# Kernel tuning notes

Hardware: AMD Instinct MI355X
Metric: run time of the kernel (lower is better)

The kernel has to match this reference:

```python
import jax, jax.numpy as jnp
import numpy as np

N = 400000      # total atoms across batch of molecules
E = 1600000     # directed edges (avg degree 4)
G = 4096        # number of graphs (molecules)
F_IN = 78       # atomic feature size
H = 128         # gnn hidden dims (gnn_0 = gnn_1 = 128)
FF0, FF1 = 256, 128


def _lin(k, fan_in, fan_out):
    return jax.random.normal(k, (fan_in, fan_out), jnp.float32) / np.sqrt(fan_in).astype(np.float32)


def setup_inputs() -> dict:
    key = jax.random.key(0)
    ks = jax.random.split(key, 10)
    x = jax.random.normal(ks[0], (N, F_IN), jnp.float32)
    edge_index = jax.random.randint(ks[1], (2, E), 0, N, dtype=jnp.int64)
    # sorted graph ids, guaranteed non-empty segments (empty segment -> -inf under max pool)
    batch = (jnp.arange(N, dtype=jnp.int64) * G) // N
    return {
        'x': x, 'edge_index': edge_index, 'batch': batch,
        'W0': _lin(ks[2], F_IN, H), 'b0': jnp.zeros((H,), jnp.float32),
        'W1': _lin(ks[3], H, H),    'b1': jnp.zeros((H,), jnp.float32),
        'Wf0': _lin(ks[4], H, FF0), 'bf0': jnp.zeros((FF0,), jnp.float32),
        'Wf1': _lin(ks[5], FF0, FF1), 'bf1': jnp.zeros((FF1,), jnp.float32),
    }


def _gcn_conv(h, W, b, src, dst, dinv):
    # GCNConv with add_self_loops=True, symmetric normalization.
    hw = h @ W                                     # [N, out]
    norm = dinv[src] * dinv[dst]                   # [E]
    msg = hw[src] * norm[:, None]                  # gather + scale
    agg = jax.ops.segment_sum(msg, dst, num_segments=h.shape[0])
    agg = agg + hw * (dinv * dinv)[:, None]        # self-loop contribution
    return agg + b


def reference(x, edge_index, batch, W0, b0, W1, b1, Wf0, bf0, Wf1, bf1):
    src, dst = edge_index[0], edge_index[1]
    # degree of A + I computed at target nodes (PyG gcn_norm uses col)
    deg = jax.ops.segment_sum(jnp.ones((E,), x.dtype), dst, num_segments=N) + 1.0
    dinv = jax.lax.rsqrt(deg)

    h = jax.nn.relu(_gcn_conv(x, W0, b0, src, dst, dinv))
    h = jax.nn.relu(_gcn_conv(h, W1, b1, src, dst, dinv))

    g = jax.ops.segment_max(h, batch, num_segments=G)   # global max pool [G, H]

    g = jax.nn.relu(g @ Wf0 + bf0)   # dropout is identity in eval
    g = jax.nn.relu(g @ Wf1 + bf1)
    return g
```

## Files before the change

kernel.cpp:

```cpp
#include <hip/hip_runtime.h>
#include <cstdint>
#include <cstddef>

#define NATOMS 400000
#define NEDGES 1600000
#define NGRAPH 4096
#define F_INN  78
#define HDIM   128
#define FF0D   256
#define FF1D   128

typedef __attribute__((ext_vector_type(8))) short short8;
typedef __attribute__((ext_vector_type(4))) short short4v;
typedef __attribute__((ext_vector_type(4))) float f32x4;
typedef __attribute__((ext_vector_type(2))) float f32x2;

static __device__ __forceinline__ short f2bf(float f) {
    unsigned u = __builtin_bit_cast(unsigned, f);
    unsigned r = (u + 0x7fffu + ((u >> 16) & 1u)) >> 16;
    return (short)r;
}
static __device__ __forceinline__ float bf2f(unsigned short u) {
    return __builtin_bit_cast(float, ((unsigned)u) << 16);
}

__global__ __launch_bounds__(256) void k_degi(const int* __restrict__ dst,
                                              int* __restrict__ deg,
                                              int* __restrict__ rank, int E) {
    int e = blockIdx.x * 256 + threadIdx.x;
    if (e < E) rank[e] = atomicAdd(&deg[dst[e]], 1);
}

__global__ __launch_bounds__(256) void k_scan1(int* __restrict__ data,
                                               int* __restrict__ blockSums,
                                               float* __restrict__ dinv, int n) {
    __shared__ int ts[256];
    const int base = blockIdx.x * 1024 + threadIdx.x * 4;
    int v[4];
    #pragma unroll
    for (int j = 0; j < 4; ++j) v[j] = (base + j < n) ? data[base + j] : 0;
    #pragma unroll
    for (int j = 0; j < 4; ++j)
        if (base + j < n) dinv[base + j] = rsqrtf((float)v[j] + 1.0f);
    const int tot = v[0] + v[1] + v[2] + v[3];
    ts[threadIdx.x] = tot;
    __syncthreads();
    #pragma unroll
    for (int off = 1; off < 256; off <<= 1) {
        int t = (threadIdx.x >= off) ? ts[threadIdx.x - off] : 0;
        __syncthreads();
        ts[threadIdx.x] += t;
        __syncthreads();
    }
    int run = ts[threadIdx.x] - tot;
    #pragma unroll
    for (int j = 0; j < 4; ++j) {
        if (base + j < n) data[base + j] = run;
        run += v[j];
    }
    if (threadIdx.x == 255) blockSums[blockIdx.x] = ts[255];
}

__global__ __launch_bounds__(512) void k_scan2(int* __restrict__ blockSums, int nb) {
    __shared__ int ts[512];
    int v = (threadIdx.x < nb) ? blockSums[threadIdx.x] : 0;
    ts[threadIdx.x] = v;
    __syncthreads();
    #pragma unroll
    for (int off = 1; off < 512; off <<= 1) {
        int t = (threadIdx.x >= off) ? ts[threadIdx.x - off] : 0;
        __syncthreads();
        ts[threadIdx.x] += t;
        __syncthreads();
    }
    if (threadIdx.x < nb) blockSums[threadIdx.x] = ts[threadIdx.x] - v;
}

__global__ __launch_bounds__(256) void k_scan3(int* __restrict__ data,
                                               const int* __restrict__ blockSums,
                                               int n, int total) {
    const int off = blockSums[blockIdx.x];
    const int base = blockIdx.x * 1024 + threadIdx.x * 4;
    #pragma unroll
    for (int j = 0; j < 4; ++j)
        if (base + j < n) data[base + j] += off;
    if (blockIdx.x == 0 && threadIdx.x == 0) data[n] = total;
}

__global__ __launch_bounds__(256) void k_fill(const int* __restrict__ src,
                                              const int* __restrict__ dst,
                                              const int* __restrict__ row_start,
                                              const int* __restrict__ rank,
                                              int2* __restrict__ csr_ev,
                                              const float* __restrict__ dinv, int E) {
    int e = blockIdx.x * 256 + threadIdx.x;
    if (e >= E) return;
    int d = dst[e];
    int s = src[e];
    int pos = row_start[d] + rank[e];
    float norm = dinv[s] * dinv[d];
    csr_ev[pos] = make_int2(s, __builtin_bit_cast(int, norm));
}

template<int KC, int KSRC>
__global__ __launch_bounds__(64) void k_packw(const float* __restrict__ W,
                                              short* __restrict__ wf) {
    int t = blockIdx.x * 64 + threadIdx.x;
    int f = t >> 6, lane = t & 63;
    int ct = f / KC, kc = f % KC;
    int n  = ct * 16 + (lane & 15);
    int k0 = kc * 32 + (lane >> 4) * 8;
    short8 o;
    #pragma unroll
    for (int j = 0; j < 8; ++j) {
        int k = k0 + j;
        float v = (k < KSRC) ? W[(size_t)k * 128 + n] : 0.f;
        o[j] = f2bf(v);
    }
    *(short8*)(wf + (size_t)t * 8) = o;
}

template<int KC, bool F32IN, int KSRC>
__global__ __launch_bounds__(256) void k_gemm_mfma(
    const void* __restrict__ inv, const short* __restrict__ wfrag,
    short* __restrict__ outp, int M)
{
    constexpr int NFRAG = 8 * KC;
    __shared__ short lds_w[NFRAG * 64 * 8];
    __shared__ __align__(16) char lds_st[4 * 4096];

    const int tid = threadIdx.x;
    #pragma unroll
    for (int it = 0; it < NFRAG * 64 / 256; ++it) {
        int t = it * 256 + tid;
        *(short8*)(lds_w + (size_t)t * 8) = *(const short8*)(wfrag + (size_t)t * 8);
    }
    __syncthreads();

    const int lane = tid & 63;
    const int m = lane & 15, q = lane >> 4;
    const int wid = tid >> 6;
    const int gw = blockIdx.x * 4 + wid;
    const int NW = gridDim.x * 4;
    const int NTILE = M / 16;
    char* const st = lds_st + wid * 4096;

    auto tile_mma = [&](int t, const short8* afr) {
        f32x4 acc[8];
        #pragma unroll
        for (int ct = 0; ct < 8; ++ct) acc[ct] = (f32x4){0.f, 0.f, 0.f, 0.f};
        #pragma unroll
        for (int kc = 0; kc < KC; ++kc)
            #pragma unroll
            for (int ct = 0; ct < 8; ++ct) {
                const short8 wv = *(const short8*)(lds_w + ((size_t)((ct * KC + kc) * 64 + lane)) * 8);
                acc[ct] = __builtin_amdgcn_mfma_f32_16x16x32_bf16(wv, afr[kc], acc[ct], 0, 0, 0);
            }
        #pragma unroll
        for (int ct = 0; ct < 8; ++ct) {
            short4v o;
            o.x = f2bf(acc[ct][0]);
            o.y = f2bf(acc[ct][1]);
            o.z = f2bf(acc[ct][2]);
            o.w = f2bf(acc[ct][3]);
            const int c = (ct * 32 + q * 8) ^ ((m & 7) << 4);
            *(short4v*)(st + m * 256 + c) = o;
        }
        #pragma unroll
        for (int p = 0; p < 4; ++p) {
            const int r = p * 4 + (lane >> 4);
            const int c = ((lane & 15) * 16) ^ ((r & 7) << 4);
            const short8 v = *(const short8*)(st + r * 256 + c);
            *(short8*)(outp + (size_t)(t * 16 + r) * 128 + (lane & 15) * 8) = v;
        }
    };

    if constexpr (F32IN) {
        float raw[KC][8];
        short8 afr[KC];
        auto load_raw = [&](int tile) {
            const float* xr = (const float*)inv + (size_t)(tile * 16 + m) * KSRC;
            #pragma unroll
            for (int kc = 0; kc < KC; ++kc) {
                const int k0 = kc * 32 + q * 8;
                #pragma unroll
                for (int p = 0; p < 4; ++p) {
                    const int k = k0 + 2 * p;
                    if (k + 2 <= KSRC) {
                        f32x2 tv = *(const f32x2*)(xr + k);
                        raw[kc][2 * p] = tv.x; raw[kc][2 * p + 1] = tv.y;
                    } else {
                        raw[kc][2 * p] = 0.f; raw[kc][2 * p + 1] = 0.f;
                    }
                }
            }
        };
        auto cvt = [&]() {
            #pragma unroll
            for (int kc = 0; kc < KC; ++kc) {
                short8 a;
                #pragma unroll
                for (int j = 0; j < 8; ++j) a[j] = f2bf(raw[kc][j]);
                afr[kc] = a;
            }
        };

        load_raw(gw);
        for (int t = gw; t < NTILE; t += NW) {
            cvt();
            const int tn = t + NW;
            if (tn < NTILE) load_raw(tn);
            tile_mma(t, afr);
        }
    } else {
        short8 fA[KC], fB[KC];
        auto load_to = [&](int tile, short8* b) {
            const short* xr = (const short*)inv + (size_t)(tile * 16 + m) * KSRC;
            #pragma unroll
            for (int kc = 0; kc < KC; ++kc)
                b[kc] = *(const short8*)(xr + kc * 32 + q * 8);
        };

        load_to(gw, fA);
        for (int t = gw; t < NTILE; t += NW) {
            const int tn = t + NW;
            if (tn < NTILE) load_to(tn, fB);
            tile_mma(t, fA);
            #pragma unroll
            for (int kc = 0; kc < KC; ++kc) fA[kc] = fB[kc];
        }
    }
}

template<bool POOL>
__global__ __launch_bounds__(256) void k_gather_half(
    const unsigned short* __restrict__ hw, unsigned short* __restrict__ agg,
    const int* __restrict__ row_start, const int2* __restrict__ csr_ev,
    const float* __restrict__ dinv, const float* __restrict__ bias,
    const int* __restrict__ batch, int* __restrict__ pool, int half)
{
    const int n  = blockIdx.x * 32 + (threadIdx.x >> 3);
    const int c8 = half * 64 + (threadIdx.x & 7) * 8;
    const float dv = dinv[n];
    const float d2 = dv * dv;

    float acc[8];
    {
        const short8 sv = *(const short8*)(hw + (size_t)n * HDIM + c8);
        #pragma unroll
        for (int j = 0; j < 8; ++j)
            acc[j] = fmaf(bf2f((unsigned short)sv[j]), d2, bias[c8 + j]);
    }

    const int s0 = row_start[n], s1 = row_start[n + 1];
    int i = s0;
    for (; i + 3 < s1; i += 4) {
        const int2 e0 = csr_ev[i];
        const int2 e1 = csr_ev[i + 1];
        const int2 e2 = csr_ev[i + 2];
        const int2 e3 = csr_ev[i + 3];
        const short8 r0 = *(const short8*)(hw + (size_t)e0.x * HDIM + c8);
        const short8 r1 = *(const short8*)(hw + (size_t)e1.x * HDIM + c8);
        const short8 r2 = *(const short8*)(hw + (size_t)e2.x * HDIM + c8);
        const short8 r3 = *(const short8*)(hw + (size_t)e3.x * HDIM + c8);
        const float w0 = __builtin_bit_cast(float, e0.y);
        const float w1 = __builtin_bit_cast(float, e1.y);
        const float w2 = __builtin_bit_cast(float, e2.y);
        const float w3 = __builtin_bit_cast(float, e3.y);
        #pragma unroll
        for (int j = 0; j < 8; ++j) acc[j] = fmaf(bf2f((unsigned short)r0[j]), w0, acc[j]);
        #pragma unroll
        for (int j = 0; j < 8; ++j) acc[j] = fmaf(bf2f((unsigned short)r1[j]), w1, acc[j]);
        #pragma unroll
        for (int j = 0; j < 8; ++j) acc[j] = fmaf(bf2f((unsigned short)r2[j]), w2, acc[j]);
        #pragma unroll
        for (int j = 0; j < 8; ++j) acc[j] = fmaf(bf2f((unsigned short)r3[j]), w3, acc[j]);
    }
    for (; i < s1; ++i) {
        const int2 e0 = csr_ev[i];
        const short8 r0 = *(const short8*)(hw + (size_t)e0.x * HDIM + c8);
        const float w0 = __builtin_bit_cast(float, e0.y);
        #pragma unroll
        for (int j = 0; j < 8; ++j) acc[j] = fmaf(bf2f((unsigned short)r0[j]), w0, acc[j]);
    }

    if constexpr (!POOL) {
        short8 o;
        #pragma unroll
        for (int j = 0; j < 8; ++j) o[j] = f2bf(fmaxf(acc[j], 0.f));
        __builtin_nontemporal_store(o, (short8*)(agg + (size_t)n * HDIM + c8));
    } else {
        const int gbase = batch[blockIdx.x * 32];
        const int glast = batch[blockIdx.x * 32 + 31];
        const int idx   = batch[n] - gbase;

        float red[2][8];
        #pragma unroll
        for (int s = 0; s < 2; ++s)
            #pragma unroll
            for (int j = 0; j < 8; ++j)
                red[s][j] = (idx == s) ? fmaxf(acc[j], 0.f) : 0.f;

        #pragma unroll
        for (int msk = 8; msk <= 32; msk <<= 1)
            #pragma unroll
            for (int s = 0; s < 2; ++s)
                #pragma unroll
                for (int j = 0; j < 8; ++j)
                    red[s][j] = fmaxf(red[s][j], __shfl_xor(red[s][j], msk));

        __shared__ float sm[4][2][64];
        const int wid  = threadIdx.x >> 6;
        const int lane = threadIdx.x & 63;
        if (lane < 8) {
            #pragma unroll
            for (int s = 0; s < 2; ++s)
                #pragma unroll
                for (int j = 0; j < 8; ++j)
                    sm[wid][s][lane * 8 + j] = red[s][j];
        }
        __syncthreads();
        if (threadIdx.x < 128) {
            const int s = threadIdx.x >> 6;
            const int f = threadIdx.x & 63;
            if (s == 0 || glast != gbase) {
                float m = fmaxf(fmaxf(sm[0][s][f], sm[1][s][f]),
                                fmaxf(sm[2][s][f], sm[3][s][f]));
                atomicMax(pool + (size_t)(gbase + s) * HDIM + half * 64 + f,
                          __builtin_bit_cast(int, m));
            }
        }
    }
}

template<int K, int NC, bool OUT_RELU_BIAS>
__global__ __launch_bounds__(256) void k_gemm(
    const float* __restrict__ in, const float* __restrict__ W,
    const float* __restrict__ out_bias, float* __restrict__ out0, int M)
{
    constexpr int BK = 32;
    constexpr int TC = NC / 8;
    constexpr int TR = 256 / TC;
    constexpr int ROWS = TR * 8;
    constexpr int XST = ROWS + 4;

    __shared__ float xs[BK][XST];
    __shared__ float ws[BK][NC];

    const int tid = threadIdx.x;
    const int tc  = tid % TC;
    const int tr  = tid / TC;
    const int row0 = blockIdx.x * ROWS;

    float acc[8][8];
    #pragma unroll
    for (int i = 0; i < 8; ++i)
        #pragma unroll
        for (int j = 0; j < 8; ++j) acc[i][j] = 0.f;

    for (int k0 = 0; k0 < K; k0 += BK) {
        {
            constexpr int TASKS = BK * NC / 4;
            #pragma unroll
            for (int it = 0; it < TASKS / 256; ++it) {
                int t  = it * 256 + tid;
                int wk = t / (NC / 4);
                int wc = (t % (NC / 4)) * 4;
                *(float4*)(&ws[wk][wc]) = *(const float4*)(W + (size_t)(k0 + wk) * NC + wc);
            }
        }
        {
            constexpr int TASKS = ROWS * BK / 4;
            #pragma unroll
            for (int it = 0; it < TASKS / 256; ++it) {
                int t   = it * 256 + tid;
                int r   = t / (BK / 4);
                int kq  = (t % (BK / 4)) * 4;
                float4 x4 = *(const float4*)(in + (size_t)(row0 + r) * K + k0 + kq);
                xs[kq + 0][r] = x4.x; xs[kq + 1][r] = x4.y;
                xs[kq + 2][r] = x4.z; xs[kq + 3][r] = x4.w;
            }
        }
        __syncthreads();
        #pragma unroll 8
        for (int kk = 0; kk < BK; ++kk) {
            float a[8], b[8];
            #pragma unroll
            for (int i = 0; i < 8; ++i) a[i] = xs[kk][tr * 8 + i];
            #pragma unroll
            for (int j = 0; j < 8; ++j) b[j] = ws[kk][tc * 8 + j];
            #pragma unroll
            for (int i = 0; i < 8; ++i)
                #pragma unroll
                for (int j = 0; j < 8; ++j)
                    acc[i][j] = fmaf(a[i], b[j], acc[i][j]);
        }
        __syncthreads();
    }

    #pragma unroll
    for (int i = 0; i < 8; ++i) {
        const int row = row0 + tr * 8 + i;
        #pragma unroll
        for (int jq = 0; jq < 2; ++jq) {
            const int col = tc * 8 + jq * 4;
            float4 v;
            v.x = acc[i][jq * 4 + 0]; v.y = acc[i][jq * 4 + 1];
            v.z = acc[i][jq * 4 + 2]; v.w = acc[i][jq * 4 + 3];
            if constexpr (OUT_RELU_BIAS) {
                const float4 bb = *(const float4*)(out_bias + col);
                v.x = fmaxf(v.x + bb.x, 0.f); v.y = fmaxf(v.y + bb.y, 0.f);
                v.z = fmaxf(v.z + bb.z, 0.f); v.w = fmaxf(v.w + bb.w, 0.f);
            }
            *(float4*)(out0 + (size_t)row * NC + col) = v;
        }
    }
}

extern "C" void kernel_launch(void* const* d_in, const int* in_sizes, int n_in,
                              void* d_out, int out_size, void* d_ws, size_t ws_size,
                              hipStream_t stream) {
    const float* x    = (const float*)d_in[0];
    const int*   ei   = (const int*)d_in[1];
    const int*   batch= (const int*)d_in[2];
    const float* W0   = (const float*)d_in[3];
    const float* b0   = (const float*)d_in[4];
    const float* W1   = (const float*)d_in[5];
    const float* b1   = (const float*)d_in[6];
    const float* Wf0  = (const float*)d_in[7];
    const float* bf0  = (const float*)d_in[8];
    const float* Wf1  = (const float*)d_in[9];
    const float* bf1  = (const float*)d_in[10];
    float* out = (float*)d_out;

    const int* srcI = ei;
    const int* dstI = ei + NEDGES;

    constexpr int SCAN_NBLK = (NATOMS + 1023) / 1024;

    char* base = (char*)d_ws;
    unsigned short* hwA  = (unsigned short*)(base + 0);
    unsigned short* aggB = (unsigned short*)(base + 102400000);
    int*   rank      = (int*)(base + 102400000);
    float* dinv      = (float*)(base + 204800000);
    int*   row_start = (int*)(base + 206400000);
    int2*  csr_ev    = (int2*)(base + 208000064);
    int*   blockSums = (int*)(base + 220800064);
    float* pool      = (float*)(base + 220802112);
    float* ff0       = (float*)(base + 222899264);
    short* wf0       = (short*)(base + 227093568);
    short* wf1       = (short*)(base + 227118144);

    hipMemsetAsync(row_start, 0, (size_t)(NATOMS + 1) * sizeof(int), stream);
    hipMemsetAsync(pool, 0, (size_t)NGRAPH * HDIM * sizeof(float), stream);
    k_degi<<<(NEDGES + 255) / 256, 256, 0, stream>>>(dstI, row_start, rank, NEDGES);
    k_scan1<<<SCAN_NBLK, 256, 0, stream>>>(row_start, blockSums, dinv, NATOMS);
    k_scan2<<<1, 512, 0, stream>>>(blockSums, SCAN_NBLK);
    k_scan3<<<SCAN_NBLK, 256, 0, stream>>>(row_start, blockSums, NATOMS, NEDGES);
    k_fill<<<(NEDGES + 255) / 256, 256, 0, stream>>>(srcI, dstI, row_start, rank,
                                                     csr_ev, dinv, NEDGES);

    k_packw<3, F_INN><<<8 * 3, 64, 0, stream>>>(W0, wf0);
    k_packw<4, HDIM><<<8 * 4, 64, 0, stream>>>(W1, wf1);

    k_gemm_mfma<3, true, F_INN><<<1024, 256, 0, stream>>>(x, wf0, (short*)hwA, NATOMS);
    k_gather_half<false><<<NATOMS / 32, 256, 0, stream>>>(hwA, aggB, row_start, csr_ev,
                                                          dinv, b0, nullptr, nullptr, 0);
    k_gather_half<false><<<NATOMS / 32, 256, 0, stream>>>(hwA, aggB, row_start, csr_ev,
                                                          dinv, b0, nullptr, nullptr, 1);

    k_gemm_mfma<4, false, HDIM><<<1024, 256, 0, stream>>>(aggB, wf1, (short*)hwA, NATOMS);
    k_gather_half<true><<<NATOMS / 32, 256, 0, stream>>>(hwA, nullptr, row_start, csr_ev,
                                                         dinv, b1, batch, (int*)pool, 0);
    k_gather_half<true><<<NATOMS / 32, 256, 0, stream>>>(hwA, nullptr, row_start, csr_ev,
                                                         dinv, b1, batch, (int*)pool, 1);

    k_gemm<HDIM, FF0D, true><<<NGRAPH / 64, 256, 0, stream>>>(pool, Wf0, bf0, ff0, NGRAPH);
    k_gemm<FF0D, FF1D, true><<<NGRAPH / 128, 256, 0, stream>>>(ff0, Wf1, bf1, out, NGRAPH);
}
```

Baseline: 661.1 us.

## Aggregate raw 78-dim features before first GEMM and fold bias into weights

Layer 0 now aggregates first and transforms second, using (A·X)·W instead of A·(X·W). Input features are packed to bf16 with an 80-wide row. A single gather over that narrower row replaces the two 64-column half-gathers over 128-dim hidden rows. A constant-one column is written into the padding slot, so the bias becomes an extra weight row, and ReLU is fused into the MFMA GEMM epilogue. This reduces gather bandwidth for the first layer, at the cost of an extra pack kernel and rounding the aggregation inputs to bf16 before the matmul.

```diff
diff --git a/kernel.cpp b/kernel.cpp
--- a/kernel.cpp
+++ b/kernel.cpp
@@ -9,6 +9,8 @@
 #define HDIM   128
 #define FF0D   256
 #define FF1D   128
+
+#define XPAD   80
 
 typedef __attribute__((ext_vector_type(8))) short short8;
 typedef __attribute__((ext_vector_type(4))) short short4v;
@@ -102,8 +104,9 @@
     csr_ev[pos] = make_int2(s, __builtin_bit_cast(int, norm));
 }
 
-template<int KC, int KSRC>
+template<int KC, int KSRC, bool BIASROW>
 __global__ __launch_bounds__(64) void k_packw(const float* __restrict__ W,
+                                              const float* __restrict__ b,
                                               short* __restrict__ wf) {
     int t = blockIdx.x * 64 + threadIdx.x;
     int f = t >> 6, lane = t & 63;
@@ -114,15 +117,117 @@
     #pragma unroll
     for (int j = 0; j < 8; ++j) {
         int k = k0 + j;
-        float v = (k < KSRC) ? W[(size_t)k * 128 + n] : 0.f;
+        float v = 0.f;
+        if (k < KSRC) v = W[(size_t)k * 128 + n];
+        else if (BIASROW && k == KSRC) v = b[n];
         o[j] = f2bf(v);
     }
     *(short8*)(wf + (size_t)t * 8) = o;
 }
 
-template<int KC, bool F32IN, int KSRC>
+__global__ __launch_bounds__(256) void k_packx(const float* __restrict__ x,
+                                               unsigned short* __restrict__ xb) {
+    int t = blockIdx.x * 256 + threadIdx.x;
+    if (t >= NATOMS * 20) return;
+    int n = t / 20, g = t % 20;
+    const float* xr = x + (size_t)n * F_INN + g * 4;
+    short4v o;
+    if (g < 19) {
+        f32x2 a = *(const f32x2*)(xr);
+        f32x2 b = *(const f32x2*)(xr + 2);
+        o.x = f2bf(a.x); o.y = f2bf(a.y); o.z = f2bf(b.x); o.w = f2bf(b.y);
+    } else {
+        f32x2 a = *(const f32x2*)(xr);
+        o.x = f2bf(a.x); o.y = f2bf(a.y); o.z = 0; o.w = 0;
+    }
+    *(short4v*)(xb + (size_t)n * XPAD + g * 4) = o;
+}
+
+__global__ __launch_bounds__(256) void k_gather78(
+    const unsigned short* __restrict__ xb, unsigned short* __restrict__ aggx,
+    const int* __restrict__ row_start, const int2* __restrict__ csr_ev,
+    const float* __restrict__ dinv)
+{
+    const int n  = blockIdx.x * 32 + (threadIdx.x >> 3);
+    const int l  = threadIdx.x & 7;
+    const int c8 = l * 8;
+    const int ct = 64 + l * 2;
+    const float dv = dinv[n];
+    const float d2 = dv * dv;
+
+    float acc[8], tacc0, tacc1;
+    {
+        const short8 sv = *(const short8*)(xb + (size_t)n * XPAD + c8);
+        const unsigned tv = *(const unsigned*)(xb + (size_t)n * XPAD + ct);
+        #pragma unroll
+        for (int j = 0; j < 8; ++j) acc[j] = bf2f((unsigned short)sv[j]) * d2;
+        tacc0 = bf2f((unsigned short)(tv & 0xffff)) * d2;
+        tacc1 = bf2f((unsigned short)(tv >> 16)) * d2;
+    }
+
+    const int s0 = row_start[n], s1 = row_start[n + 1];
+    int i = s0;
+    for (; i + 3 < s1; i += 4) {
+        const int2 e0 = csr_ev[i];
+        const int2 e1 = csr_ev[i + 1];
+        const int2 e2 = csr_ev[i + 2];
+        const int2 e3 = csr_ev[i + 3];
+        const short8 r0 = *(const short8*)(xb + (size_t)e0.x * XPAD + c8);
+        const short8 r1 = *(const short8*)(xb + (size_t)e1.x * XPAD + c8);
+        const short8 r2 = *(const short8*)(xb + (size_t)e2.x * XPAD + c8);
+        const short8 r3 = *(const short8*)(xb + (size_t)e3.x * XPAD + c8);
+        const unsigned t0 = *(const unsigned*)(xb + (size_t)e0.x * XPAD + ct);
+        const unsigned t1 = *(const unsigned*)(xb + (size_t)e1.x * XPAD + ct);
+        const unsigned t2 = *(const unsigned*)(xb + (size_t)e2.x * XPAD + ct);
+        const unsigned t3 = *(const unsigned*)(xb + (size_t)e3.x * XPAD + ct);
+        const float w0 = __builtin_bit_cast(float, e0.y);
+        const float w1 = __builtin_bit_cast(float, e1.y);
+        const float w2 = __builtin_bit_cast(float, e2.y);
+        const float w3 = __builtin_bit_cast(float, e3.y);
+        #pragma unroll
+        for (int j = 0; j < 8; ++j) acc[j] = fmaf(bf2f((unsigned short)r0[j]), w0, acc[j]);
+        #pragma unroll
+        for (int j = 0; j < 8; ++j) acc[j] = fmaf(bf2f((unsigned short)r1[j]), w1, acc[j]);
+        #pragma unroll
+        for (int j = 0; j < 8; ++j) acc[j] = fmaf(bf2f((unsigned short)r2[j]), w2, acc[j]);
+        #pragma unroll
+        for (int j = 0; j < 8; ++j) acc[j] = fmaf(bf2f((unsigned short)r3[j]), w3, acc[j]);
+        tacc0 = fmaf(bf2f((unsigned short)(t0 & 0xffff)), w0, tacc0);
+        tacc1 = fmaf(bf2f((unsigned short)(t0 >> 16)),    w0, tacc1);
+        tacc0 = fmaf(bf2f((unsigned short)(t1 & 0xffff)), w1, tacc0);
+        tacc1 = fmaf(bf2f((unsigned short)(t1 >> 16)),    w1, tacc1);
+        tacc0 = fmaf(bf2f((unsigned short)(t2 & 0xffff)), w2, tacc0);
+        tacc1 = fmaf(bf2f((unsigned short)(t2 >> 16)),    w2, tacc1);
+        tacc0 = fmaf(bf2f((unsigned short)(t3 & 0xffff)), w3, tacc0);
+        tacc1 = fmaf(bf2f((unsigned short)(t3 >> 16)),    w3, tacc1);
+    }
+    for (; i < s1; ++i) {
+        const int2 e0 = csr_ev[i];
+        const short8 r0 = *(const short8*)(xb + (size_t)e0.x * XPAD + c8);
+        const unsigned t0 = *(const unsigned*)(xb + (size_t)e0.x * XPAD + ct);
+        const float w0 = __builtin_bit_cast(float, e0.y);
+        #pragma unroll
+        for (int j = 0; j < 8; ++j) acc[j] = fmaf(bf2f((unsigned short)r0[j]), w0, acc[j]);
+        tacc0 = fmaf(bf2f((unsigned short)(t0 & 0xffff)), w0, tacc0);
+        tacc1 = fmaf(bf2f((unsigned short)(t0 >> 16)),    w0, tacc1);
+    }
+
+    short8 o;
+    #pragma unroll
+    for (int j = 0; j < 8; ++j) o[j] = f2bf(acc[j]);
+    *(short8*)(aggx + (size_t)n * XPAD + c8) = o;
+    unsigned to;
+    if (l == 7) to = 0x00003F80u;
+    else {
+        to = (unsigned)(unsigned short)f2bf(tacc0) |
+             ((unsigned)(unsigned short)f2bf(tacc1) << 16);
+    }
+    *(unsigned*)(aggx + (size_t)n * XPAD + ct) = to;
+}
+
+template<int KC, int KSRC, bool RELU>
 __global__ __launch_bounds__(256) void k_gemm_mfma(
-    const void* __restrict__ inv, const short* __restrict__ wfrag,
+    const short* __restrict__ inv, const short* __restrict__ wfrag,
     short* __restrict__ outp, int M)
 {
     constexpr int NFRAG = 8 * KC;
@@ -159,10 +264,12 @@
         #pragma unroll
         for (int ct = 0; ct < 8; ++ct) {
             short4v o;
-            o.x = f2bf(acc[ct][0]);
-            o.y = f2bf(acc[ct][1]);
-            o.z = f2bf(acc[ct][2]);
-            o.w = f2bf(acc[ct][3]);
+            float v0 = acc[ct][0], v1 = acc[ct][1], v2 = acc[ct][2], v3 = acc[ct][3];
+            if constexpr (RELU) {
+                v0 = fmaxf(v0, 0.f); v1 = fmaxf(v1, 0.f);
+                v2 = fmaxf(v2, 0.f); v3 = fmaxf(v3, 0.f);
+            }
+            o.x = f2bf(v0); o.y = f2bf(v1); o.z = f2bf(v2); o.w = f2bf(v3);
             const int c = (ct * 32 + q * 8) ^ ((m & 7) << 4);
             *(short4v*)(st + m * 256 + c) = o;
         }
@@ -175,66 +282,30 @@
         }
     };
 
-    if constexpr (F32IN) {
-        float raw[KC][8];
-        short8 afr[KC];
-        auto load_raw = [&](int tile) {
-            const float* xr = (const float*)inv + (size_t)(tile * 16 + m) * KSRC;
-            #pragma unroll
-            for (int kc = 0; kc < KC; ++kc) {
-                const int k0 = kc * 32 + q * 8;
-                #pragma unroll
-                for (int p = 0; p < 4; ++p) {
-                    const int k = k0 + 2 * p;
-                    if (k + 2 <= KSRC) {
-                        f32x2 tv = *(const f32x2*)(xr + k);
-                        raw[kc][2 * p] = tv.x; raw[kc][2 * p + 1] = tv.y;
-                    } else {
-                        raw[kc][2 * p] = 0.f; raw[kc][2 * p + 1] = 0.f;
-                    }
-                }
-            }
-        };
-        auto cvt = [&]() {
-            #pragma unroll
-            for (int kc = 0; kc < KC; ++kc) {
-                short8 a;
-                #pragma unroll
-                for (int j = 0; j < 8; ++j) a[j] = f2bf(raw[kc][j]);
-                afr[kc] = a;
-            }
-        };
-
-        load_raw(gw);
-        for (int t = gw; t < NTILE; t += NW) {
-            cvt();
-            const int tn = t + NW;
-            if (tn < NTILE) load_raw(tn);
-            tile_mma(t, afr);
-        }
-    } else {
-        short8 fA[KC], fB[KC];
-        auto load_to = [&](int tile, short8* b) {
-            const short* xr = (const short*)inv + (size_t)(tile * 16 + m) * KSRC;
-            #pragma unroll
-            for (int kc = 0; kc < KC; ++kc)
-                b[kc] = *(const short8*)(xr + kc * 32 + q * 8);
-        };
-
-        load_to(gw, fA);
-        for (int t = gw; t < NTILE; t += NW) {
-            const int tn = t + NW;
-            if (tn < NTILE) load_to(tn, fB);
-            tile_mma(t, fA);
-            #pragma unroll
-            for (int kc = 0; kc < KC; ++kc) fA[kc] = fB[kc];
-        }
-    }
-}
-
-template<bool POOL>
-__global__ __launch_bounds__(256) void k_gather_half(
-    const unsigned short* __restrict__ hw, unsigned short* __restrict__ agg,
+    short8 fA[KC], fB[KC];
+    auto load_to = [&](int tile, short8* b) {
+        const short* xr = inv + (size_t)(tile * 16 + m) * KSRC;
+        #pragma unroll
+        for (int kc = 0; kc < KC; ++kc) {
+            const int k0 = kc * 32 + q * 8;
+            short8 v = {0, 0, 0, 0, 0, 0, 0, 0};
+            if (k0 + 8 <= KSRC) v = *(const short8*)(xr + k0);
+            b[kc] = v;
+        }
+    };
+
+    load_to(gw, fA);
+    for (int t = gw; t < NTILE; t += NW) {
+        const int tn = t + NW;
+        if (tn < NTILE) load_to(tn, fB);
+        tile_mma(t, fA);
+        #pragma unroll
+        for (int kc = 0; kc < KC; ++kc) fA[kc] = fB[kc];
+    }
+}
+
+__global__ __launch_bounds__(256) void k_gather_pool(
+    const unsigned short* __restrict__ hw,
     const int* __restrict__ row_start, const int2* __restrict__ csr_ev,
     const float* __restrict__ dinv, const float* __restrict__ bias,
     const int* __restrict__ batch, int* __restrict__ pool, int half)
@@ -284,51 +355,44 @@
         for (int j = 0; j < 8; ++j) acc[j] = fmaf(bf2f((unsigned short)r0[j]), w0, acc[j]);
     }
 
-    if constexpr (!POOL) {
-        short8 o;
-        #pragma unroll
-        for (int j = 0; j < 8; ++j) o[j] = f2bf(fmaxf(acc[j], 0.f));
-        __builtin_nontemporal_store(o, (short8*)(agg + (size_t)n * HDIM + c8));
-    } else {
-        const int gbase = batch[blockIdx.x * 32];
-        const int glast = batch[blockIdx.x * 32 + 31];
-        const int idx   = batch[n] - gbase;
-
-        float red[2][8];
+    const int gbase = batch[blockIdx.x * 32];
+    const int glast = batch[blockIdx.x * 32 + 31];
+    const int idx   = batch[n] - gbase;
+
+    float red[2][8];
+    #pragma unroll
+    for (int s = 0; s < 2; ++s)
+        #pragma unroll
+        for (int j = 0; j < 8; ++j)
+            red[s][j] = (idx == s) ? fmaxf(acc[j], 0.f) : 0.f;
+
+    #pragma unroll
+    for (int msk = 8; msk <= 32; msk <<= 1)
         #pragma unroll
         for (int s = 0; s < 2; ++s)
             #pragma unroll
             for (int j = 0; j < 8; ++j)
-                red[s][j] = (idx == s) ? fmaxf(acc[j], 0.f) : 0.f;
-
-        #pragma unroll
-        for (int msk = 8; msk <= 32; msk <<= 1)
-            #pragma unroll
-            for (int s = 0; s < 2; ++s)
-                #pragma unroll
-                for (int j = 0; j < 8; ++j)
-                    red[s][j] = fmaxf(red[s][j], __shfl_xor(red[s][j], msk));
-
-        __shared__ float sm[4][2][64];
-        const int wid  = threadIdx.x >> 6;
-        const int lane = threadIdx.x & 63;
-        if (lane < 8) {
-            #pragma unroll
-            for (int s = 0; s < 2; ++s)
-                #pragma unroll
-                for (int j = 0; j < 8; ++j)
-                    sm[wid][s][lane * 8 + j] = red[s][j];
-        }
-        __syncthreads();
-        if (threadIdx.x < 128) {
-            const int s = threadIdx.x >> 6;
-            const int f = threadIdx.x & 63;
-            if (s == 0 || glast != gbase) {
-                float m = fmaxf(fmaxf(sm[0][s][f], sm[1][s][f]),
-                                fmaxf(sm[2][s][f], sm[3][s][f]));
-                atomicMax(pool + (size_t)(gbase + s) * HDIM + half * 64 + f,
-                          __builtin_bit_cast(int, m));
-            }
+                red[s][j] = fmaxf(red[s][j], __shfl_xor(red[s][j], msk));
+
+    __shared__ float sm[4][2][64];
+    const int wid  = threadIdx.x >> 6;
+    const int lane = threadIdx.x & 63;
+    if (lane < 8) {
+        #pragma unroll
+        for (int s = 0; s < 2; ++s)
+            #pragma unroll
+            for (int j = 0; j < 8; ++j)
+                sm[wid][s][lane * 8 + j] = red[s][j];
+    }
+    __syncthreads();
+    if (threadIdx.x < 128) {
+        const int s = threadIdx.x >> 6;
+        const int f = threadIdx.x & 63;
+        if (s == 0 || glast != gbase) {
+            float m = fmaxf(fmaxf(sm[0][s][f], sm[1][s][f]),
+                            fmaxf(sm[2][s][f], sm[3][s][f]));
+            atomicMax(pool + (size_t)(gbase + s) * HDIM + half * 64 + f,
+                      __builtin_bit_cast(int, m));
         }
     }
 }
@@ -440,7 +504,9 @@
 
     char* base = (char*)d_ws;
     unsigned short* hwA  = (unsigned short*)(base + 0);
+    unsigned short* aggx = (unsigned short*)(base + 0);
     unsigned short* aggB = (unsigned short*)(base + 102400000);
+    unsigned short* xb   = (unsigned short*)(base + 102400000);
     int*   rank      = (int*)(base + 102400000);
     float* dinv      = (float*)(base + 204800000);
     int*   row_start = (int*)(base + 206400000);
@@ -460,20 +526,20 @@
     k_fill<<<(NEDGES + 255) / 256, 256, 0, stream>>>(srcI, dstI, row_start, rank,
                                                      csr_ev, dinv, NEDGES);
 
-    k_packw<3, F_INN><<<8 * 3, 64, 0, stream>>>(W0, wf0);
-    k_packw<4, HDIM><<<8 * 4, 64, 0, stream>>>(W1, wf1);
-
-    k_gemm_mfma<3, true, F_INN><<<1024, 256, 0, stream>>>(x, wf0, (short*)hwA, NATOMS);
-    k_gather_half<false><<<NATOMS / 32, 256, 0, stream>>>(hwA, aggB, row_start, csr_ev,
-                                                          dinv, b0, nullptr, nullptr, 0);
-    k_gather_half<false><<<NATOMS / 32, 256, 0, stream>>>(hwA, aggB, row_start, csr_ev,
-                                                          dinv, b0, nullptr, nullptr, 1);
-
-    k_gemm_mfma<4, false, HDIM><<<1024, 256, 0, stream>>>(aggB, wf1, (short*)hwA, NATOMS);
-    k_gather_half<true><<<NATOMS / 32, 256, 0, stream>>>(hwA, nullptr, row_start, csr_ev,
-                                                         dinv, b1, batch, (int*)pool, 0);
-    k_gather_half<true><<<NATOMS / 32, 256, 0, stream>>>(hwA, nullptr, row_start, csr_ev,
-                                                         dinv, b1, batch, (int*)pool, 1);
+    k_packw<3, F_INN, true><<<8 * 3, 64, 0, stream>>>(W0, b0, wf0);
+    k_packw<4, HDIM, false><<<8 * 4, 64, 0, stream>>>(W1, nullptr, wf1);
+    k_packx<<<(NATOMS * 20 + 255) / 256, 256, 0, stream>>>(x, xb);
+
+    k_gather78<<<NATOMS / 32, 256, 0, stream>>>(xb, aggx, row_start, csr_ev, dinv);
+    k_gemm_mfma<3, XPAD, true><<<1024, 256, 0, stream>>>((const short*)aggx, wf0,
+                                                         (short*)aggB, NATOMS);
+
+    k_gemm_mfma<4, HDIM, false><<<1024, 256, 0, stream>>>((const short*)aggB, wf1,
+                                                          (short*)hwA, NATOMS);
+    k_gather_pool<<<NATOMS / 32, 256, 0, stream>>>(hwA, row_start, csr_ev,
+                                                   dinv, b1, batch, (int*)pool, 0);
+    k_gather_pool<<<NATOMS / 32, 256, 0, stream>>>(hwA, row_start, csr_ev,
+                                                   dinv, b1, batch, (int*)pool, 1);
 
     k_gemm<HDIM, FF0D, true><<<NGRAPH / 64, 256, 0, stream>>>(pool, Wf0, bf0, ff0, NGRAPH);
     k_gemm<FF0D, FF1D, true><<<NGRAPH / 128, 256, 0, stream>>>(ff0, Wf1, bf1, out, NGRAPH);
```

New measurement: 650.1 us. No clear change (-1.7%).
